# Kernel tuning notes

Hardware: AMD Instinct MI355X
Metric: run time of the kernel (lower is better)

The kernel has to match this reference:

```python
import jax, jax.numpy as jnp
import numpy as np

IMG_H, IMG_W = 800.0, 1280.0
STRIDE = 16
SCALE = 1.0 / STRIDE
P, S = 14, 1              # pooler resolution, sampling ratio
NUM_CLASSES = 80
BBOX_W = (10.0, 10.0, 5.0, 5.0)
SCORE_TH, NMS_TH, MAX_DET, IOU_TH = 0.05, 0.5, 100, 0.5
SCALE_CLAMP = float(np.log(1000.0 / 16.0))


def _make_boxes(key, n_img, n_box):
    k1, k2, k3, k4 = jax.random.split(key, 4)
    x1 = jax.random.uniform(k1, (n_img, n_box)) * (IMG_W - 64.0)
    y1 = jax.random.uniform(k2, (n_img, n_box)) * (IMG_H - 64.0)
    w = jax.random.uniform(k3, (n_img, n_box)) * 300.0 + 16.0
    h = jax.random.uniform(k4, (n_img, n_box)) * 300.0 + 16.0
    x2 = jnp.minimum(x1 + w, IMG_W)
    y2 = jnp.minimum(y1 + h, IMG_H)
    return jnp.stack([x1, y1, x2, y2], axis=-1)


def setup_inputs() -> dict:
    key = jax.random.key(0)
    ks = jax.random.split(key, 6)
    features = jax.random.normal(ks[0], (2, 50, 80, 1024), dtype=jnp.float32)
    proposals = _make_boxes(ks[1], 2, 256)
    gt_boxes = _make_boxes(ks[2], 2, 64)
    gt_classes = jax.random.randint(ks[3], (2, 64), 0, NUM_CLASSES)
    W_cls = jax.random.normal(ks[4], (1024, NUM_CLASSES + 1), dtype=jnp.float32) * 0.01
    b_cls = jnp.zeros((NUM_CLASSES + 1,), jnp.float32)
    W_box = jax.random.normal(ks[5], (1024, 4), dtype=jnp.float32) * 0.01
    b_box = jnp.zeros((4,), jnp.float32)
    return {"features": features, "proposals": proposals, "gt_boxes": gt_boxes,
            "gt_classes": gt_classes, "W_cls": W_cls, "b_cls": b_cls,
            "W_box": W_box, "b_box": b_box}


def pairwise_iou(a, b):
    # a: [G,4], b: [R,4], boxes as (x1,y1,x2,y2) -> [G,R]
    area_a = (a[:, 2] - a[:, 0]) * (a[:, 3] - a[:, 1])
    area_b = (b[:, 2] - b[:, 0]) * (b[:, 3] - b[:, 1])
    lt = jnp.maximum(a[:, None, :2], b[None, :, :2])
    rb = jnp.minimum(a[:, None, 2:], b[None, :, 2:])
    wh = jnp.clip(rb - lt, 0.0)
    inter = wh[..., 0] * wh[..., 1]
    return inter / jnp.maximum(area_a[:, None] + area_b[None, :] - inter, 1e-9)


def roi_align_one(feat, boxes):
    # feat: [H,W,C], boxes: [R,4] in image coords -> pooled [R,P,P,C]
    H, W, C = feat.shape
    b = boxes * SCALE
    x1, y1, x2, y2 = b[:, 0], b[:, 1], b[:, 2], b[:, 3]
    off = (jnp.arange(S, dtype=feat.dtype) + 0.5) / S       # [S]
    grid = jnp.arange(P, dtype=feat.dtype)                   # [P]
    bh = ((y2 - y1) / P)[:, None, None]
    bw = ((x2 - x1) / P)[:, None, None]
    # aligned RoIAlign sample coords (half-pixel offset)
    gy = y1[:, None, None] + (grid[None, :, None] + off[None, None, :]) * bh - 0.5  # [R,P,S]
    gx = x1[:, None, None] + (grid[None, :, None] + off[None, None, :]) * bw - 0.5
    gy = jnp.clip(gy, 0.0, H - 1.0)
    gx = jnp.clip(gx, 0.0, W - 1.0)
    y0 = jnp.floor(gy); x0 = jnp.floor(gx)
    y0i = y0.astype(jnp.int32); x0i = x0.astype(jnp.int32)
    y1i = jnp.minimum(y0i + 1, H - 1); x1i = jnp.minimum(x0i + 1, W - 1)
    ly = gy - y0; lx = gx - x0

    def g(yi, xi):  # cross-product gather -> [R,P,S,P,S,C]
        return feat[yi[:, :, :, None, None], xi[:, None, None, :, :]]

    wy0 = (1.0 - ly)[:, :, :, None, None, None]; wy1 = ly[:, :, :, None, None, None]
    wx0 = (1.0 - lx)[:, None, None, :, :, None]; wx1 = lx[:, None, None, :, :, None]
    val = wy0 * (wx0 * g(y0i, x0i) + wx1 * g(y0i, x1i)) \
        + wy1 * (wx0 * g(y1i, x0i) + wx1 * g(y1i, x1i))
    return val.mean(axis=(2, 4))  # average sampling points per bin -> [R,P,P,C]


def decode_boxes(deltas, boxes):
    wx, wy, ww, wh = BBOX_W
    widths = boxes[..., 2] - boxes[..., 0]
    heights = boxes[..., 3] - boxes[..., 1]
    ctr_x = boxes[..., 0] + 0.5 * widths
    ctr_y = boxes[..., 1] + 0.5 * heights
    dx = deltas[..., 0] / wx
    dy = deltas[..., 1] / wy
    dw = jnp.minimum(deltas[..., 2] / ww, SCALE_CLAMP)
    dh = jnp.minimum(deltas[..., 3] / wh, SCALE_CLAMP)
    pcx = dx * widths + ctr_x
    pcy = dy * heights + ctr_y
    pw = jnp.exp(dw) * widths
    ph = jnp.exp(dh) * heights
    out = jnp.stack([pcx - 0.5 * pw, pcy - 0.5 * ph, pcx + 0.5 * pw, pcy + 0.5 * ph], axis=-1)
    lim = jnp.array([IMG_W, IMG_H, IMG_W, IMG_H], out.dtype)
    return jnp.clip(out, 0.0, lim)


def nms_keep(boxes, scores):
    # greedy class-agnostic NMS, fixed-size keep mask [R]
    R = scores.shape[0]
    order = jnp.argsort(-scores)
    sb = boxes[order]
    iou = pairwise_iou(sb, sb)
    idx = jnp.arange(R)

    def body(i, keep):
        suppressed = jnp.any((idx < i) & keep & (iou[:, i] > NMS_TH))
        return keep.at[i].set(jnp.logical_not(suppressed))

    keep_sorted = jax.lax.fori_loop(0, R, body, jnp.ones((R,), bool))
    return jnp.zeros((R,), bool).at[order].set(keep_sorted)


def reference(features, proposals, gt_boxes, gt_classes, W_cls, b_cls, W_box, b_box):
    N, R = proposals.shape[:2]
    # --- proposal <-> gt matching (training-side labeling) ---
    iou_m = jax.vmap(pairwise_iou)(gt_boxes, proposals)          # [N,G,R]
    matched_vals = iou_m.max(axis=1)
    matched_idxs = iou_m.argmax(axis=1)                          # [N,R]
    match_labels = (matched_vals >= IOU_TH).astype(jnp.int32)    # [N,R] fg=1/bg=0
    # --- RoIAlign pooling on the single C4 feature map ---
    pooled = jax.vmap(roi_align_one)(features, proposals)        # [N,R,P,P,C]
    feat_vec = pooled.mean(axis=(2, 3))                          # res5 surrogate global avg -> [N,R,C]
    # --- box predictor ---
    scores_all = jax.nn.softmax(feat_vec @ W_cls + b_cls, axis=-1)
    fg_scores = scores_all[..., :NUM_CLASSES].max(axis=-1)       # drop background column
    deltas = feat_vec @ W_box + b_box
    boxes = decode_boxes(deltas, proposals)                      # [N,R,4]
    # --- score threshold + NMS + top-k ---
    keep = jax.vmap(nms_keep)(boxes, fg_scores) & (fg_scores > SCORE_TH)
    masked = jnp.where(keep, fg_scores, -jnp.inf)
    rank = jnp.argsort(jnp.argsort(-masked, axis=-1), axis=-1)
    keep = keep & (rank < MAX_DET)
    det = jnp.concatenate([boxes, fg_scores[..., None], keep.astype(boxes.dtype)[..., None]], axis=-1)
    return det, matched_idxs, match_labels
```

## Files before the change

### kernel.cpp

```cpp
#include <hip/hip_runtime.h>
#include <math.h>

#define N_IMG 2
#define R_PROP 256
#define G_GT 64
#define C_CH 1024
#define FH 50
#define FW 80
#define P_POOL 14
#define NCLS 80
#define IMG_W_F 1280.0f
#define IMG_H_F 800.0f
#define SCALE_F 0.0625f
#define SCORE_TH_F 0.05f
#define NMS_TH_F 0.5f
#define IOU_TH_F 0.5f
#define MAX_DET_I 100
#define SCALE_CLAMP_F 4.135166556742356f

__global__ __launch_bounds__(512) void prep_kernel(
    const float* __restrict__ proposals,
    const float* __restrict__ gt_boxes,
    int* __restrict__ perm,
    float* __restrict__ out_idx,
    float* __restrict__ out_lbl) {
  const int t = threadIdx.x;
  const int n = t >> 8;
  __shared__ float cy[N_IMG * R_PROP];
  const float* pb = proposals + (size_t)t * 4;
  float bx1 = pb[0], by1 = pb[1], bx2 = pb[2], by2 = pb[3];
  cy[t] = by1 + by2;
  __syncthreads();

  {
    float my = cy[t];
    int rk = 0;
    const int base = n * R_PROP;
#pragma unroll 8
    for (int j = base; j < base + R_PROP; ++j) {
      float cj = cy[j];
      rk += (cj < my) || (cj == my && j < t);
    }
    perm[base + rk] = t & 255;
  }

  {
    float area_b = (bx2 - bx1) * (by2 - by1);
    float best = -1.0f;
    int bidx = 0;
    const float* gt = gt_boxes + (size_t)n * G_GT * 4;
#pragma unroll 4
    for (int g = 0; g < G_GT; ++g) {
      float gx1 = gt[g * 4 + 0], gy1 = gt[g * 4 + 1];
      float gx2 = gt[g * 4 + 2], gy2 = gt[g * 4 + 3];
      float area_a = (gx2 - gx1) * (gy2 - gy1);
      float ix1 = fmaxf(gx1, bx1), iy1 = fmaxf(gy1, by1);
      float ix2 = fminf(gx2, bx2), iy2 = fminf(gy2, by2);
      float iw = fmaxf(ix2 - ix1, 0.0f), ih = fmaxf(iy2 - iy1, 0.0f);
      float inter = iw * ih;
      float iou = inter / fmaxf(area_a + area_b - inter, 1e-9f);
      if (iou > best) { best = iou; bidx = g; }
    }
    out_idx[t] = (float)bidx;
    out_lbl[t] = (best >= IOU_TH_F) ? 1.0f : 0.0f;
  }
}

__global__ __launch_bounds__(1024) void roihead_kernel(
    const float* __restrict__ features,
    const float* __restrict__ proposals,
    const int* __restrict__ perm,
    const float* __restrict__ W_cls,
    const float* __restrict__ W_box,
    const float* __restrict__ b_cls,
    const float* __restrict__ b_box,
    float* __restrict__ boxes_dec,
    float* __restrict__ scores) {
  const int b = blockIdx.x;
  const int xcd = b & 7;
  const int slot = b >> 3;
  const int n = xcd >> 2;
  const int band = xcd & 3;
  const int blk = n * R_PROP + perm[n * R_PROP + band * 64 + slot];

  const float* feat = features + (size_t)n * (FH * FW * C_CH);
  const int t = threadIdx.x;
  const int c4 = t & 255;
  const int g = t >> 8;

  __shared__ float s_Wy[FH];
  __shared__ float s_Wx[FW];
  __shared__ int s_b[4];
  __shared__ float4 s_red[3][256];
  __shared__ __align__(16) float sf[C_CH];
  __shared__ float s_part[12][85];
  __shared__ float sl[85];
  __shared__ float s_red2[8];

  if (t < FH) s_Wy[t] = 0.0f;
  if (t >= 128 && t < 128 + FW) s_Wx[t - 128] = 0.0f;
  __syncthreads();

  if (t < 2 * P_POOL) {
    const float* pb = proposals + (size_t)blk * 4;
    bool isY = t < P_POOL;
    int i = isY ? t : t - P_POOL;
    float lo = isY ? pb[1] : pb[0];
    float hi = isY ? pb[3] : pb[2];
    float limit = isY ? (float)(FH - 1) : (float)(FW - 1);
    float b1 = lo * SCALE_F, b2 = hi * SCALE_F;
    float bs = (b2 - b1) * (1.0f / P_POOL);
    float gg = b1 + ((float)i + 0.5f) * bs - 0.5f;
    gg = fminf(fmaxf(gg, 0.0f), limit);
    float fl = floorf(gg);
    int i0 = (int)fl;
    int i1 = min(i0 + 1, (int)limit);
    float l = gg - fl;
    if (isY) {
      atomicAdd(&s_Wy[i0], 1.0f - l);
      atomicAdd(&s_Wy[i1], l);
      if (i == 0) s_b[0] = i0;
      if (i == P_POOL - 1) s_b[1] = i1;
    } else {
      atomicAdd(&s_Wx[i0], 1.0f - l);
      atomicAdd(&s_Wx[i1], l);
      if (i == 0) s_b[2] = i0;
      if (i == P_POOL - 1) s_b[3] = i1;
    }
  }
  __syncthreads();

  {
    const int ylo = s_b[0], yhi = s_b[1], xlo = s_b[2], xhi = s_b[3];
    float4 acc = make_float4(0.f, 0.f, 0.f, 0.f);
    for (int y = ylo + g; y <= yhi; y += 4) {
      float wy = s_Wy[y];
      const float4* row = (const float4*)(feat + (size_t)y * (FW * C_CH)) + c4;
#pragma unroll 8
      for (int x = xlo; x <= xhi; ++x) {
        float w = wy * s_Wx[x];
        float4 f = row[x * (C_CH / 4)];
        acc.x += w * f.x;
        acc.y += w * f.y;
        acc.z += w * f.z;
        acc.w += w * f.w;
      }
    }
    if (g > 0) s_red[g - 1][c4] = acc;
    __syncthreads();
    if (g == 0) {
      const float inv = 1.0f / (float)(P_POOL * P_POOL);
#pragma unroll
      for (int p = 0; p < 3; ++p) {
        float4 a = s_red[p][c4];
        acc.x += a.x; acc.y += a.y; acc.z += a.z; acc.w += a.w;
      }
      ((float4*)sf)[c4] =
          make_float4(acc.x * inv, acc.y * inv, acc.z * inv, acc.w * inv);
    }
    __syncthreads();
  }

  {
    const int kq = t / 85;
    const int j = t - kq * 85;
    if (kq < 12) {
      float acc = 0.0f;
      if (j < 81) {
        const float* __restrict__ w = W_cls + j;
#pragma unroll 8
        for (int k = kq; k < C_CH; k += 12) acc += sf[k] * w[k * 81];
      } else {
        const float* __restrict__ w = W_box + (j - 81);
#pragma unroll 8
        for (int k = kq; k < C_CH; k += 12) acc += sf[k] * w[k * 4];
      }
      s_part[kq][j] = acc;
    }
  }
  __syncthreads();

  if (t < 85) {
    float bias = (t < 81) ? b_cls[t] : b_box[t - 81];
    float acc = bias;
#pragma unroll
    for (int p = 0; p < 12; ++p) acc += s_part[p][t];
    sl[t] = acc;
  }
  __syncthreads();

  if (t < 128) {
    float xm = (t < 81) ? sl[t] : -INFINITY;
    float xf = (t < NCLS) ? sl[t] : -INFINITY;
#pragma unroll
    for (int off = 32; off; off >>= 1) {
      xm = fmaxf(xm, __shfl_down(xm, off, 64));
      xf = fmaxf(xf, __shfl_down(xf, off, 64));
    }
    if ((t & 63) == 0) { s_red2[t >> 6] = xm; s_red2[2 + (t >> 6)] = xf; }
  }
  __syncthreads();
  if (t < 128) {
    const float m = fmaxf(s_red2[0], s_red2[1]);
    float xs = (t < 81) ? expf(sl[t] - m) : 0.0f;
#pragma unroll
    for (int off = 32; off; off >>= 1) xs += __shfl_down(xs, off, 64);
    if ((t & 63) == 0) s_red2[4 + (t >> 6)] = xs;
  }
  __syncthreads();

  if (t == 0) {
    const float m = fmaxf(s_red2[0], s_red2[1]);
    float sum = s_red2[4] + s_red2[5];
    float fgm = fmaxf(s_red2[2], s_red2[3]);
    scores[blk] = expf(fgm - m) / sum;

    const float* pb = proposals + (size_t)blk * 4;
    float w = pb[2] - pb[0], h = pb[3] - pb[1];
    float cx = pb[0] + 0.5f * w, cyc = pb[1] + 0.5f * h;
    float dx = sl[81] * 0.1f;
    float dy = sl[82] * 0.1f;
    float dw = fminf(sl[83] * 0.2f, SCALE_CLAMP_F);
    float dh = fminf(sl[84] * 0.2f, SCALE_CLAMP_F);
    float pcx = dx * w + cx, pcy = dy * h + cyc;
    float pw = expf(dw) * w, ph = expf(dh) * h;
    float ox1 = fminf(fmaxf(pcx - 0.5f * pw, 0.0f), IMG_W_F);
    float oy1 = fminf(fmaxf(pcy - 0.5f * ph, 0.0f), IMG_H_F);
    float ox2 = fminf(fmaxf(pcx + 0.5f * pw, 0.0f), IMG_W_F);
    float oy2 = fminf(fmaxf(pcy + 0.5f * ph, 0.0f), IMG_H_F);
    float* bd = boxes_dec + (size_t)blk * 4;
    bd[0] = ox1; bd[1] = oy1; bd[2] = ox2; bd[3] = oy2;
  }
}

__global__ __launch_bounds__(1024) void nms_kernel(
    const float* __restrict__ boxes_dec,
    const float* __restrict__ scores,
    float* __restrict__ det) {
  const int n = blockIdx.x;
  const int u = threadIdx.x;
  const int i = u & 255;
  const int q = u >> 8;
  const int j40 = q * 16;

  __shared__ __align__(16) float ss[R_PROP];
  __shared__ float4 sbs[R_PROP];
  __shared__ int s_part[4 * R_PROP];
  __shared__ int s_rank[R_PROP];
  __shared__ __align__(16) unsigned long long s_mask[R_PROP * 4];
  __shared__ unsigned long long s_keep[4];
  __shared__ __align__(16) float sm[R_PROP];

  float4 myb;
  float mys;
  if (q == 0) {
    myb = ((const float4*)boxes_dec)[n * R_PROP + i];
    mys = scores[n * R_PROP + i];
    ss[i] = mys;
  }
  __syncthreads();

  {
    float s = ss[i];
    int cnt = 0;
#pragma unroll
    for (int j4 = j40; j4 < j40 + 16; ++j4) {
      float4 v = ((const float4*)ss)[j4];
      int jb = j4 * 4;
      cnt += (v.x > s) || (v.x == s && jb + 0 < i);
      cnt += (v.y > s) || (v.y == s && jb + 1 < i);
      cnt += (v.z > s) || (v.z == s && jb + 2 < i);
      cnt += (v.w > s) || (v.w == s && jb + 3 < i);
    }
    s_part[q * R_PROP + i] = cnt;
  }
  __syncthreads();
  if (q == 0) {
    int rk = s_part[i] + s_part[R_PROP + i] + s_part[2 * R_PROP + i] +
             s_part[3 * R_PROP + i];
    s_rank[i] = rk;
    sbs[rk] = myb;
  }
  __syncthreads();

  {
    float4 bi = sbs[i];
    float area_i = (bi.z - bi.x) * (bi.w - bi.y);
    unsigned long long m = 0;
    const int j0 = q * 64;
#pragma unroll 8
    for (int jj = 0; jj < 64; ++jj) {
      float4 bj = sbs[j0 + jj];
      float area_j = (bj.z - bj.x) * (bj.w - bj.y);
      float ix1 = fmaxf(bi.x, bj.x), iy1 = fmaxf(bi.y, bj.y);
      float ix2 = fminf(bi.z, bj.z), iy2 = fminf(bi.w, bj.w);
      float iw = fmaxf(ix2 - ix1, 0.0f), ih = fmaxf(iy2 - iy1, 0.0f);
      float inter = iw * ih;
      float iou = inter / fmaxf(area_i + area_j - inter, 1e-9f);
      m |= (iou > NMS_TH_F) ? (1ull << jj) : 0ull;
    }
    s_mask[i * 4 + q] = m;
  }
  __syncthreads();

  if (u == 0) {
    unsigned long long K0 = ~0ull, K1 = ~0ull, K2 = ~0ull, K3 = ~0ull;
#pragma unroll 16
    for (int b = 1; b < 64; ++b) {
      unsigned long long m0 = s_mask[(size_t)b * 4 + 0];
      unsigned long long sup = m0 & K0 & ((1ull << b) - 1ull);
      K0 = sup ? (K0 & ~(1ull << b)) : K0;
    }
#pragma unroll 16
    for (int b = 0; b < 64; ++b) {
      const unsigned long long* mi = &s_mask[(size_t)(64 + b) * 4];
      unsigned long long m0 = mi[0], m1 = mi[1];
      unsigned long long sup = (m0 & K0) | (m1 & K1 & ((1ull << b) - 1ull));
      K1 = sup ? (K1 & ~(1ull << b)) : K1;
    }
#pragma unroll 16
    for (int b = 0; b < 64; ++b) {
      const unsigned long long* mi = &s_mask[(size_t)(128 + b) * 4];
      unsigned long long m0 = mi[0], m1 = mi[1], m2 = mi[2];
      unsigned long long sup =
          (m0 & K0) | (m1 & K1) | (m2 & K2 & ((1ull << b) - 1ull));
      K2 = sup ? (K2 & ~(1ull << b)) : K2;
    }
#pragma unroll 16
    for (int b = 0; b < 64; ++b) {
      const unsigned long long* mi = &s_mask[(size_t)(192 + b) * 4];
      unsigned long long m0 = mi[0], m1 = mi[1], m2 = mi[2], m3 = mi[3];
      unsigned long long sup = (m0 & K0) | (m1 & K1) | (m2 & K2) |
                               (m3 & K3 & ((1ull << b) - 1ull));
      K3 = sup ? (K3 & ~(1ull << b)) : K3;
    }
    s_keep[0] = K0; s_keep[1] = K1; s_keep[2] = K2; s_keep[3] = K3;
  }
  __syncthreads();

  bool kept = false;
  if (q == 0) {
    int rk = s_rank[i];
    kept = ((s_keep[rk >> 6] >> (rk & 63)) & 1ull) && (mys > SCORE_TH_F);
    sm[i] = kept ? mys : -INFINITY;
  }
  __syncthreads();

  {
    float mym = sm[i];
    int cnt = 0;
#pragma unroll
    for (int j4 = j40; j4 < j40 + 16; ++j4) {
      float4 v = ((const float4*)sm)[j4];
      int jb = j4 * 4;
      cnt += (v.x > mym) || (v.x == mym && jb + 0 < i);
      cnt += (v.y > mym) || (v.y == mym && jb + 1 < i);
      cnt += (v.z > mym) || (v.z == mym && jb + 2 < i);
      cnt += (v.w > mym) || (v.w == mym && jb + 3 < i);
    }
    s_part[q * R_PROP + i] = cnt;
  }
  __syncthreads();

  if (q == 0) {
    int rk2 = s_part[i] + s_part[R_PROP + i] + s_part[2 * R_PROP + i] +
              s_part[3 * R_PROP + i];
    kept = kept && (rk2 < MAX_DET_I);
    float* dr = det + ((size_t)n * R_PROP + i) * 6;
    dr[0] = myb.x; dr[1] = myb.y; dr[2] = myb.z; dr[3] = myb.w;
    dr[4] = mys;
    dr[5] = kept ? 1.0f : 0.0f;
  }
}

extern "C" void kernel_launch(void* const* d_in, const int* in_sizes, int n_in,
                              void* d_out, int out_size, void* d_ws, size_t ws_size,
                              hipStream_t stream) {
  const float* features  = (const float*)d_in[0];
  const float* proposals = (const float*)d_in[1];
  const float* gt_boxes  = (const float*)d_in[2];
  const float* W_cls = (const float*)d_in[4];
  const float* b_cls = (const float*)d_in[5];
  const float* W_box = (const float*)d_in[6];
  const float* b_box = (const float*)d_in[7];

  float* out = (float*)d_out;
  float* out_det = out;
  float* out_idx = out + N_IMG * R_PROP * 6;
  float* out_lbl = out_idx + N_IMG * R_PROP;

  float* boxes_dec = (float*)d_ws;
  float* scores    = boxes_dec + (size_t)N_IMG * R_PROP * 4;
  int*   perm      = (int*)(scores + N_IMG * R_PROP);

  prep_kernel<<<1, 512, 0, stream>>>(proposals, gt_boxes, perm, out_idx, out_lbl);
  roihead_kernel<<<N_IMG * R_PROP, 1024, 0, stream>>>(
      features, proposals, perm, W_cls, W_box, b_cls, b_box, boxes_dec, scores);
  nms_kernel<<<N_IMG, 1024, 0, stream>>>(boxes_dec, scores, out_det);
}
```

Before: 167.5 us.

## Split RoIAlign into per-row tasks with a dynamic work queue and finalize pass

Replaces the one-block-per-proposal RoIAlign with a row-granular task list built in prep_kernel. A persistent roi_rows_kernel pulls (proposal, y) tasks from an atomic counter and writes per-row partial sums to a workspace buffer. A separate finalize kernel reduces the rows and runs the predictor. The aim is to balance the uneven per-proposal work across CUs. The cost is an extra kernel launch, a large intermediate buffer written and read through global memory, and serial prefix sums in the single-block prep kernel.

```diff
diff --git a/kernel.cpp b/kernel.cpp
--- a/kernel.cpp
+++ b/kernel.cpp
@@ -17,19 +17,29 @@
 #define IOU_TH_F 0.5f
 #define MAX_DET_I 100
 #define SCALE_CLAMP_F 4.135166556742356f
+#define TASK_CAP 11264
 
 __global__ __launch_bounds__(512) void prep_kernel(
     const float* __restrict__ proposals,
     const float* __restrict__ gt_boxes,
-    int* __restrict__ perm,
+    int* __restrict__ off,
+    int* __restrict__ sblk,
+    int* __restrict__ task_p,
+    int* __restrict__ task_y,
+    float* __restrict__ task_wy,
+    int* __restrict__ counter,
     float* __restrict__ out_idx,
     float* __restrict__ out_lbl) {
   const int t = threadIdx.x;
   const int n = t >> 8;
   __shared__ float cy[N_IMG * R_PROP];
+  __shared__ int s_sblk[N_IMG * R_PROP];
+  __shared__ int s_nr[N_IMG * R_PROP];
+
   const float* pb = proposals + (size_t)t * 4;
   float bx1 = pb[0], by1 = pb[1], bx2 = pb[2], by2 = pb[3];
   cy[t] = by1 + by2;
+  if (t == 0) counter[0] = 0;
   __syncthreads();
 
   {
@@ -41,7 +51,51 @@
       float cj = cy[j];
       rk += (cj < my) || (cj == my && j < t);
     }
-    perm[base + rk] = t & 255;
+    s_sblk[base + rk] = t;
+  }
+  __syncthreads();
+
+  const int p = s_sblk[t];
+  int ylo, nr;
+  float b1y, bsy;
+  {
+    float py1 = proposals[(size_t)p * 4 + 1];
+    float py2 = proposals[(size_t)p * 4 + 3];
+    b1y = py1 * SCALE_F;
+    float b2y = py2 * SCALE_F;
+    bsy = (b2y - b1y) * (1.0f / P_POOL);
+    float g0  = fminf(fmaxf(b1y + 0.5f  * bsy - 0.5f, 0.0f), (float)(FH - 1));
+    float g13 = fminf(fmaxf(b1y + 13.5f * bsy - 0.5f, 0.0f), (float)(FH - 1));
+    ylo = (int)floorf(g0);
+    int yhi = min((int)floorf(g13) + 1, FH - 1);
+    nr = yhi - ylo + 1;
+    s_nr[t] = nr;
+  }
+  __syncthreads();
+
+  int o = 0;
+  for (int j = 0; j < t; ++j) o += s_nr[j];
+  off[t] = o;
+  if (t == N_IMG * R_PROP - 1) off[N_IMG * R_PROP] = o + nr;
+  sblk[t] = p;
+
+  for (int r = 0; r < nr; ++r) {
+    int y = ylo + r;
+    float wy = 0.0f;
+#pragma unroll
+    for (int i = 0; i < P_POOL; ++i) {
+      float gg = b1y + ((float)i + 0.5f) * bsy - 0.5f;
+      gg = fminf(fmaxf(gg, 0.0f), (float)(FH - 1));
+      float fl = floorf(gg);
+      int i0 = (int)fl;
+      int i1 = min(i0 + 1, FH - 1);
+      float l = gg - fl;
+      wy += (i0 == y) ? (1.0f - l) : 0.0f;
+      wy += (i1 == y) ? l : 0.0f;
+    }
+    task_p[o + r] = p;
+    task_y[o + r] = y;
+    task_wy[o + r] = wy;
   }
 
   {
@@ -66,100 +120,101 @@
   }
 }
 
-__global__ __launch_bounds__(1024) void roihead_kernel(
+__global__ __launch_bounds__(256) void roi_rows_kernel(
     const float* __restrict__ features,
     const float* __restrict__ proposals,
-    const int* __restrict__ perm,
+    const int* __restrict__ task_p,
+    const int* __restrict__ task_y,
+    const float* __restrict__ task_wy,
+    const int* __restrict__ off,
+    int* __restrict__ counter,
+    float* __restrict__ rowbuf) {
+  const int t = threadIdx.x;
+  __shared__ float s_Wx[FW];
+  __shared__ int s_xb[2];
+  __shared__ int s_tid;
+  const int total = off[N_IMG * R_PROP];
+
+  for (;;) {
+    __syncthreads();
+    if (t < FW) s_Wx[t] = 0.0f;
+    if (t == 0) s_tid = atomicAdd(counter, 1);
+    __syncthreads();
+    const int tid = s_tid;
+    if (tid >= total) break;
+
+    const int p = task_p[tid];
+    const int y = task_y[tid];
+    const float wy = task_wy[tid];
+
+    if (t < P_POOL) {
+      const float* pb = proposals + (size_t)p * 4;
+      float b1 = pb[0] * SCALE_F, b2 = pb[2] * SCALE_F;
+      float bs = (b2 - b1) * (1.0f / P_POOL);
+      float gg = b1 + ((float)t + 0.5f) * bs - 0.5f;
+      gg = fminf(fmaxf(gg, 0.0f), (float)(FW - 1));
+      float fl = floorf(gg);
+      int i0 = (int)fl;
+      int i1 = min(i0 + 1, FW - 1);
+      float l = gg - fl;
+      atomicAdd(&s_Wx[i0], 1.0f - l);
+      atomicAdd(&s_Wx[i1], l);
+      if (t == 0) s_xb[0] = i0;
+      if (t == P_POOL - 1) s_xb[1] = i1;
+    }
+    __syncthreads();
+
+    const int xlo = s_xb[0], xhi = s_xb[1];
+    const float4* row = (const float4*)(features +
+        (size_t)(p >> 8) * (FH * FW * C_CH) + (size_t)y * (FW * C_CH));
+    float4 acc = make_float4(0.f, 0.f, 0.f, 0.f);
+#pragma unroll 4
+    for (int x = xlo; x <= xhi; ++x) {
+      float w = wy * s_Wx[x];
+      float4 f = row[x * (C_CH / 4) + t];
+      acc.x += w * f.x;
+      acc.y += w * f.y;
+      acc.z += w * f.z;
+      acc.w += w * f.w;
+    }
+    ((float4*)rowbuf)[(size_t)tid * (C_CH / 4) + t] = acc;
+  }
+}
+
+__global__ __launch_bounds__(1024) void finalize_kernel(
+    const float* __restrict__ rowbuf,
+    const int* __restrict__ off,
+    const int* __restrict__ sblk,
+    const float* __restrict__ proposals,
     const float* __restrict__ W_cls,
     const float* __restrict__ W_box,
     const float* __restrict__ b_cls,
     const float* __restrict__ b_box,
     float* __restrict__ boxes_dec,
     float* __restrict__ scores) {
-  const int b = blockIdx.x;
-  const int xcd = b & 7;
-  const int slot = b >> 3;
-  const int n = xcd >> 2;
-  const int band = xcd & 3;
-  const int blk = n * R_PROP + perm[n * R_PROP + band * 64 + slot];
-
-  const float* feat = features + (size_t)n * (FH * FW * C_CH);
+  const int s = blockIdx.x;
   const int t = threadIdx.x;
-  const int c4 = t & 255;
-  const int g = t >> 8;
-
-  __shared__ float s_Wy[FH];
-  __shared__ float s_Wx[FW];
-  __shared__ int s_b[4];
-  __shared__ float4 s_red[3][256];
+  const int p = sblk[s];
+  const int o = off[s];
+  const int nr = off[s + 1] - o;
+
   __shared__ __align__(16) float sf[C_CH];
   __shared__ float s_part[12][85];
   __shared__ float sl[85];
   __shared__ float s_red2[8];
 
-  if (t < FH) s_Wy[t] = 0.0f;
-  if (t >= 128 && t < 128 + FW) s_Wx[t - 128] = 0.0f;
-  __syncthreads();
-
-  if (t < 2 * P_POOL) {
-    const float* pb = proposals + (size_t)blk * 4;
-    bool isY = t < P_POOL;
-    int i = isY ? t : t - P_POOL;
-    float lo = isY ? pb[1] : pb[0];
-    float hi = isY ? pb[3] : pb[2];
-    float limit = isY ? (float)(FH - 1) : (float)(FW - 1);
-    float b1 = lo * SCALE_F, b2 = hi * SCALE_F;
-    float bs = (b2 - b1) * (1.0f / P_POOL);
-    float gg = b1 + ((float)i + 0.5f) * bs - 0.5f;
-    gg = fminf(fmaxf(gg, 0.0f), limit);
-    float fl = floorf(gg);
-    int i0 = (int)fl;
-    int i1 = min(i0 + 1, (int)limit);
-    float l = gg - fl;
-    if (isY) {
-      atomicAdd(&s_Wy[i0], 1.0f - l);
-      atomicAdd(&s_Wy[i1], l);
-      if (i == 0) s_b[0] = i0;
-      if (i == P_POOL - 1) s_b[1] = i1;
-    } else {
-      atomicAdd(&s_Wx[i0], 1.0f - l);
-      atomicAdd(&s_Wx[i1], l);
-      if (i == 0) s_b[2] = i0;
-      if (i == P_POOL - 1) s_b[3] = i1;
-    }
-  }
-  __syncthreads();
-
-  {
-    const int ylo = s_b[0], yhi = s_b[1], xlo = s_b[2], xhi = s_b[3];
-    float4 acc = make_float4(0.f, 0.f, 0.f, 0.f);
-    for (int y = ylo + g; y <= yhi; y += 4) {
-      float wy = s_Wy[y];
-      const float4* row = (const float4*)(feat + (size_t)y * (FW * C_CH)) + c4;
-#pragma unroll 8
-      for (int x = xlo; x <= xhi; ++x) {
-        float w = wy * s_Wx[x];
-        float4 f = row[x * (C_CH / 4)];
-        acc.x += w * f.x;
-        acc.y += w * f.y;
-        acc.z += w * f.z;
-        acc.w += w * f.w;
-      }
-    }
-    if (g > 0) s_red[g - 1][c4] = acc;
-    __syncthreads();
-    if (g == 0) {
-      const float inv = 1.0f / (float)(P_POOL * P_POOL);
-#pragma unroll
-      for (int p = 0; p < 3; ++p) {
-        float4 a = s_red[p][c4];
-        acc.x += a.x; acc.y += a.y; acc.z += a.z; acc.w += a.w;
-      }
-      ((float4*)sf)[c4] =
-          make_float4(acc.x * inv, acc.y * inv, acc.z * inv, acc.w * inv);
-    }
-    __syncthreads();
-  }
+  if (t < C_CH / 4) {
+    const float4* rb = (const float4*)rowbuf + (size_t)o * (C_CH / 4) + t;
+    float4 a = make_float4(0.f, 0.f, 0.f, 0.f);
+    for (int r = 0; r < nr; ++r) {
+      float4 v = rb[(size_t)r * (C_CH / 4)];
+      a.x += v.x; a.y += v.y; a.z += v.z; a.w += v.w;
+    }
+    const float inv = 1.0f / (float)(P_POOL * P_POOL);
+    ((float4*)sf)[t] =
+        make_float4(a.x * inv, a.y * inv, a.z * inv, a.w * inv);
+  }
+  __syncthreads();
 
   {
     const int kq = t / 85;
@@ -184,7 +239,7 @@
     float bias = (t < 81) ? b_cls[t] : b_box[t - 81];
     float acc = bias;
 #pragma unroll
-    for (int p = 0; p < 12; ++p) acc += s_part[p][t];
+    for (int q = 0; q < 12; ++q) acc += s_part[q][t];
     sl[t] = acc;
   }
   __syncthreads();
@@ -193,9 +248,9 @@
     float xm = (t < 81) ? sl[t] : -INFINITY;
     float xf = (t < NCLS) ? sl[t] : -INFINITY;
 #pragma unroll
-    for (int off = 32; off; off >>= 1) {
-      xm = fmaxf(xm, __shfl_down(xm, off, 64));
-      xf = fmaxf(xf, __shfl_down(xf, off, 64));
+    for (int off2 = 32; off2; off2 >>= 1) {
+      xm = fmaxf(xm, __shfl_down(xm, off2, 64));
+      xf = fmaxf(xf, __shfl_down(xf, off2, 64));
     }
     if ((t & 63) == 0) { s_red2[t >> 6] = xm; s_red2[2 + (t >> 6)] = xf; }
   }
@@ -204,7 +259,7 @@
     const float m = fmaxf(s_red2[0], s_red2[1]);
     float xs = (t < 81) ? expf(sl[t] - m) : 0.0f;
 #pragma unroll
-    for (int off = 32; off; off >>= 1) xs += __shfl_down(xs, off, 64);
+    for (int off2 = 32; off2; off2 >>= 1) xs += __shfl_down(xs, off2, 64);
     if ((t & 63) == 0) s_red2[4 + (t >> 6)] = xs;
   }
   __syncthreads();
@@ -213,9 +268,9 @@
     const float m = fmaxf(s_red2[0], s_red2[1]);
     float sum = s_red2[4] + s_red2[5];
     float fgm = fmaxf(s_red2[2], s_red2[3]);
-    scores[blk] = expf(fgm - m) / sum;
-
-    const float* pb = proposals + (size_t)blk * 4;
+    scores[p] = expf(fgm - m) / sum;
+
+    const float* pb = proposals + (size_t)p * 4;
     float w = pb[2] - pb[0], h = pb[3] - pb[1];
     float cx = pb[0] + 0.5f * w, cyc = pb[1] + 0.5f * h;
     float dx = sl[81] * 0.1f;
@@ -228,7 +283,7 @@
     float oy1 = fminf(fmaxf(pcy - 0.5f * ph, 0.0f), IMG_H_F);
     float ox2 = fminf(fmaxf(pcx + 0.5f * pw, 0.0f), IMG_W_F);
     float oy2 = fminf(fmaxf(pcy + 0.5f * ph, 0.0f), IMG_H_F);
-    float* bd = boxes_dec + (size_t)blk * 4;
+    float* bd = boxes_dec + (size_t)p * 4;
     bd[0] = ox1; bd[1] = oy1; bd[2] = ox2; bd[3] = oy2;
   }
 }
@@ -389,12 +444,24 @@
   float* out_idx = out + N_IMG * R_PROP * 6;
   float* out_lbl = out_idx + N_IMG * R_PROP;
 
-  float* boxes_dec = (float*)d_ws;
-  float* scores    = boxes_dec + (size_t)N_IMG * R_PROP * 4;
-  int*   perm      = (int*)(scores + N_IMG * R_PROP);
-
-  prep_kernel<<<1, 512, 0, stream>>>(proposals, gt_boxes, perm, out_idx, out_lbl);
-  roihead_kernel<<<N_IMG * R_PROP, 1024, 0, stream>>>(
-      features, proposals, perm, W_cls, W_box, b_cls, b_box, boxes_dec, scores);
+  int*   counter = (int*)d_ws;
+  int*   off     = counter + 16;
+  int*   sblk    = off + 520;
+  int*   task_p  = sblk + 512;
+  int*   task_y  = task_p + TASK_CAP;
+  float* task_wy = (float*)(task_y + TASK_CAP);
+  float* rowbuf  = (float*)((char*)d_ws + 262144);
+  float* boxes_dec =
+      (float*)((char*)d_ws + 262144 + (size_t)TASK_CAP * C_CH * 4);
+  float* scores = boxes_dec + N_IMG * R_PROP * 4;
+
+  prep_kernel<<<1, 512, 0, stream>>>(proposals, gt_boxes, off, sblk, task_p,
+                                     task_y, task_wy, counter, out_idx, out_lbl);
+  roi_rows_kernel<<<2048, 256, 0, stream>>>(features, proposals, task_p,
+                                            task_y, task_wy, off, counter,
+                                            rowbuf);
+  finalize_kernel<<<N_IMG * R_PROP, 1024, 0, stream>>>(
+      rowbuf, off, sblk, proposals, W_cls, W_box, b_cls, b_box, boxes_dec,
+      scores);
   nms_kernel<<<N_IMG, 1024, 0, stream>>>(boxes_dec, scores, out_det);
 }
```

After: 253.9 us. +51.6%, slower.
